# Kernel tuning notes

Hardware: AMD Instinct MI355X
Metric: run time of the kernel (lower is better)

Reference implementation:

```python
import jax, jax.numpy as jnp
import numpy as np

# Enformer/Borzoi-style MHA with relative positional bias
B, T, C = 2, 1536, 1536          # batch, seq bins, input channels
H, K, V = 8, 64, 192             # heads, key_size, value_size
F = 32                           # num_position_features (borzoi, asymmetric: 2 * 16 basis)


def setup_inputs() -> dict:
    key = jax.random.key(0)
    ks = jax.random.split(key, 9)
    he = lambda fan_in: (2.0 / fan_in) ** 0.5  # he_normal scale
    return {
        "x": jax.random.normal(ks[0], (B, T, C), jnp.float32),
        "Wq": jax.random.normal(ks[1], (C, H * K), jnp.float32) * he(C),
        "Wk": jax.random.normal(ks[2], (C, H * K), jnp.float32) * he(C),
        "Wv": jax.random.normal(ks[3], (C, H * V), jnp.float32) * he(C),
        "Wr": jax.random.normal(ks[4], (F, H * K), jnp.float32) * he(F),
        "r_w_bias": jax.random.normal(ks[5], (1, H, 1, K), jnp.float32) * 0.02,
        "r_r_bias": jax.random.normal(ks[6], (1, H, 1, K), jnp.float32) * 0.02,
        "Wo": jax.random.normal(ks[7], (H * V, H * V), jnp.float32) * he(H * V),
        "bo": jnp.zeros((H * V,), jnp.float32),
    }


def positional_features(positions):
    """Borzoi central-mask basis, absolute=True, asymmetric -> [L, F]."""
    nb = F // 2
    pow_rate = np.exp(np.log(T + 1) / nb).astype(np.float32)
    center_widths = pow_rate ** jnp.arange(1, nb + 1, dtype=jnp.float32) - 1.0  # [nb]
    sign = jnp.sign(positions)
    abs_pos = jnp.abs(positions)
    emb = (center_widths[None, :] > abs_pos[:, None]).astype(jnp.float32)  # [L, nb]
    return jnp.concatenate([emb, sign[:, None] * emb], axis=-1)  # [L, 2*nb]


def relative_shift(x):
    """[B,H,T,2T-1] -> [B,H,T,T] relative-shift trick (pad, reshape, slice)."""
    b, h, t, l = x.shape
    x = jnp.pad(x, ((0, 0), (0, 0), (0, 0), (1, 0)))      # [b,h,t,l+1]
    x = x.reshape(b, h, l + 1, t)[:, :, 1:, :]             # [b,h,l,t]
    x = x.reshape(b, h, t, l)
    return x[..., :t]


def reference(x, Wq, Wk, Wv, Wr, r_w_bias, r_r_bias, Wo, bo):
    q = (x @ Wq).reshape(B, T, H, K).transpose(0, 2, 1, 3)   # [B,H,T,K]
    k = (x @ Wk).reshape(B, T, H, K).transpose(0, 2, 1, 3)
    v = (x @ Wv).reshape(B, T, H, V).transpose(0, 2, 1, 3)   # [B,H,T,V]
    q = q * (K ** -0.5)  # scaling=True

    distances = jnp.arange(-T + 1, T, dtype=jnp.float32)     # [2T-1]
    pe = positional_features(distances)                       # [2T-1, F]
    rk = (pe @ Wr).reshape(2 * T - 1, H, K)                   # [2T-1, H, K]

    content_logits = jnp.einsum('bhtk,bhsk->bhts', q + r_w_bias, k)   # [B,H,T,T]
    rel_logits = jnp.einsum('bhtk,rhk->bhtr', q + r_r_bias, rk)       # [B,H,T,2T-1]
    logits = content_logits + relative_shift(rel_logits)

    weights = jax.nn.softmax(logits, axis=-1)
    out = jnp.einsum('bhts,bhsv->bhtv', weights, v)          # [B,H,T,V]
    out = out.transpose(0, 2, 1, 3).reshape(B, T, H * V)     # [B,T,H*V]
    return out @ Wo + bo
```

## Files before the change

### kernel.cpp

```cpp
#include <hip/hip_runtime.h>
#include <hip/hip_bf16.h>

typedef __hip_bfloat16 bf16;
typedef unsigned short ushort;
typedef unsigned int uint;
typedef __attribute__((ext_vector_type(8))) short short8;
typedef __attribute__((ext_vector_type(4))) float f32x4;

#define Bsz 2
#define Tn  1536
#define Cn  1536
#define Hn  8
#define Kn  64
#define Vn  192

__device__ __forceinline__ ushort f2bs(float f) {
  union { bf16 h; ushort u; } cv;
  cv.h = __float2bfloat16(f);
  return cv.u;
}
__device__ __forceinline__ float bs2f(ushort u) {
  union { float f; uint v; } cv; cv.v = ((uint)u) << 16; return cv.f;
}

__device__ __forceinline__ void gld_lds16(const ushort* g, ushort* l) {
  __builtin_amdgcn_global_load_lds(
      (const __attribute__((address_space(1))) uint*)g,
      (__attribute__((address_space(3))) uint*)l, 16, 0, 0);
}

#define DPP_MAXSTEP(x, ctrl)                                                  \
  do {                                                                        \
    union { float f; int i; } a_, b_;                                         \
    a_.f = (x);                                                               \
    b_.i = __builtin_amdgcn_update_dpp(a_.i, a_.i, (ctrl), 0xf, 0xf, true);   \
    (x) = fmaxf((x), b_.f);                                                   \
  } while (0)

__global__ __launch_bounds__(256) void prep(
    const float* __restrict__ x,  const float* __restrict__ Wq,
    const float* __restrict__ Wk, const float* __restrict__ Wv,
    const float* __restrict__ Wo, const float* __restrict__ Wr,
    ushort* __restrict__ xb, ushort* __restrict__ Wt,
    ushort* __restrict__ Wot, ushort* __restrict__ rkdb,
    unsigned char* __restrict__ lutb) {
  const int z = blockIdx.z;
  if (z < 4) {
    if (z < 2 && blockIdx.x >= 16) return;
    const float* in = (z == 0) ? Wq : (z == 1) ? Wk : (z == 2) ? Wv : Wo;
    ushort* out = (z == 0) ? Wt : (z == 1) ? Wt + 512 * 1536
                : (z == 2) ? Wt + 1024 * 1536 : Wot;
    const int Cc = (z < 2) ? 512 : 1536;
    __shared__ float tile[32][33];
    const int bx = blockIdx.x * 32;
    const int by = blockIdx.y * 32;
    const int tx = threadIdx.x & 31, ty = threadIdx.x >> 5;
#pragma unroll
    for (int i = 0; i < 32; i += 8)
      tile[ty + i][tx] = in[(size_t)(by + ty + i) * Cc + bx + tx];
    __syncthreads();
#pragma unroll
    for (int i = 0; i < 32; i += 8)
      out[(size_t)(bx + ty + i) * 1536 + by + tx] = f2bs(tile[tx][ty + i]);
  } else if (z == 4) {
    const int n4 = 3072 * 1536 / 4;
    for (int i = (blockIdx.y * 48 + blockIdx.x) * 256 + threadIdx.x; i < n4;
         i += 2304 * 256) {
      float4 v = ((const float4*)x)[i];
      uint2 o;
      o.x = (uint)f2bs(v.x) | ((uint)f2bs(v.y) << 16);
      o.y = (uint)f2bs(v.z) | ((uint)f2bs(v.w) << 16);
      ((uint2*)xb)[i] = o;
    }
  } else {
    const int base = (blockIdx.y * 48 + blockIdx.x) * 256 + threadIdx.x;
    if (base < 8 * 40 * 64) {
      const int h = base / 2560, rem = base % 2560, u = rem >> 6, k = rem & 63;
      float acc = 0.f;
      if (u < 33) {
        const float sg = (u == 32) ? 0.f : (u < 16 ? 1.f : -1.f);
        const int c = (u == 32) ? 16 : (u < 16 ? u + 1 : u - 15);
#pragma unroll
        for (int i = 0; i < 16; i++)
          if (i >= 16 - c)
            acc += Wr[i * 512 + h * 64 + k] + sg * Wr[(16 + i) * 512 + h * 64 + k];
      }
      rkdb[h * 2560 + u * 64 + k] = f2bs(acc);
    } else if (base < 8 * 40 * 64 + 3072) {
      const int idx = base - 8 * 40 * 64;
      const int d = idx - 1535;
      const float ad = fabsf((float)d);
      int c = 0;
#pragma unroll
      for (int i = 0; i < 16; i++) {
        double cw = exp(log((double)(Tn + 1)) * (double)(i + 1) / 16.0) - 1.0;
        if ((float)cw > ad) c++;
      }
      lutb[idx] = (unsigned char)((d == 0) ? 32 : (d > 0 ? c - 1 : 15 + c));
    }
  }
}

__global__ __launch_bounds__(256) void gemm_qkv(
    const ushort* __restrict__ xb, const ushort* __restrict__ Wt,
    ushort* __restrict__ qb, ushort* __restrict__ kb, ushort* __restrict__ vtb) {
  __shared__ ushort Al[128 * 32];
  __shared__ ushort Bl[128 * 32];
  const int tid = threadIdx.x;
  const int w = tid >> 6, lane = tid & 63, quad = lane >> 4, ln = lane & 15;
  const int bm = blockIdx.y * 128, bn = blockIdx.x * 128;
  const int wm = (w & 1) * 64, wn = (w >> 1) * 64;
  f32x4 acc[4][4];
#pragma unroll
  for (int i = 0; i < 4; i++)
#pragma unroll
    for (int j = 0; j < 4; j++) acc[i][j] = (f32x4){0.f, 0.f, 0.f, 0.f};

  for (int k0 = 0; k0 < 1536; k0 += 32) {
    __syncthreads();
#pragma unroll
    for (int st = 0; st < 2; st++) {
      int idx = tid + st * 256;
      int row = idx >> 2, col = (idx & 3) * 8;
      gld_lds16(xb + (size_t)(bm + row) * 1536 + k0 + col, Al + idx * 8);
      gld_lds16(Wt + (size_t)(bn + row) * 1536 + k0 + col, Bl + idx * 8);
    }
    __syncthreads();
    short8 af[4], bfr[4];
#pragma unroll
    for (int t = 0; t < 4; t++) {
      af[t]  = *(const short8*)(Al + (wm + t * 16 + ln) * 32 + quad * 8);
      bfr[t] = *(const short8*)(Bl + (wn + t * 16 + ln) * 32 + quad * 8);
    }
#pragma unroll
    for (int mt = 0; mt < 4; mt++)
#pragma unroll
      for (int nt = 0; nt < 4; nt++)
        acc[mt][nt] = __builtin_amdgcn_mfma_f32_16x16x32_bf16(
            af[mt], bfr[nt], acc[mt][nt], 0, 0, 0);
  }

  if (bn < 512) {
#pragma unroll
    for (int mt = 0; mt < 4; mt++)
#pragma unroll
      for (int nt = 0; nt < 4; nt++)
#pragma unroll
        for (int r = 0; r < 4; r++) {
          int m = bm + wm + mt * 16 + quad * 4 + r;
          int n = bn + wn + nt * 16 + ln;
          qb[(size_t)m * 512 + n] = f2bs(acc[mt][nt][r] * 0.125f);
        }
  } else if (bn < 1024) {
#pragma unroll
    for (int mt = 0; mt < 4; mt++)
#pragma unroll
      for (int nt = 0; nt < 4; nt++)
#pragma unroll
        for (int r = 0; r < 4; r++) {
          int m = bm + wm + mt * 16 + quad * 4 + r;
          int n = bn - 512 + wn + nt * 16 + ln;
          kb[(size_t)m * 512 + n] = f2bs(acc[mt][nt][r]);
        }
  } else {
#pragma unroll
    for (int mt = 0; mt < 4; mt++)
#pragma unroll
      for (int nt = 0; nt < 4; nt++) {
        int vcol = bn - 1024 + wn + nt * 16 + ln;
        int m0 = bm + wm + mt * 16 + quad * 4;
        uint2 val;
        val.x = (uint)f2bs(acc[mt][nt][0]) | ((uint)f2bs(acc[mt][nt][1]) << 16);
        val.y = (uint)f2bs(acc[mt][nt][2]) | ((uint)f2bs(acc[mt][nt][3]) << 16);
        *(uint2*)(vtb + (size_t)vcol * 3072 + m0) = val;
      }
  }
}

__global__ __launch_bounds__(256) void gemm_out(
    const ushort* __restrict__ att, const ushort* __restrict__ Wot,
    const float* __restrict__ bo, float* __restrict__ out) {
  __shared__ ushort Al[128 * 32];
  __shared__ ushort Bl[128 * 32];
  const int tid = threadIdx.x;
  const int w = tid >> 6, lane = tid & 63, quad = lane >> 4, ln = lane & 15;
  const int bm = blockIdx.y * 128, bn = blockIdx.x * 128;
  const int wm = (w & 1) * 64, wn = (w >> 1) * 64;
  f32x4 acc[4][4];
#pragma unroll
  for (int i = 0; i < 4; i++)
#pragma unroll
    for (int j = 0; j < 4; j++) acc[i][j] = (f32x4){0.f, 0.f, 0.f, 0.f};

  for (int k0 = 0; k0 < 1536; k0 += 32) {
    __syncthreads();
#pragma unroll
    for (int st = 0; st < 2; st++) {
      int idx = tid + st * 256;
      int row = idx >> 2, col = (idx & 3) * 8;
      gld_lds16(att + (size_t)(bm + row) * 1536 + k0 + col, Al + idx * 8);
      gld_lds16(Wot + (size_t)(bn + row) * 1536 + k0 + col, Bl + idx * 8);
    }
    __syncthreads();
    short8 af[4], bfr[4];
#pragma unroll
    for (int t = 0; t < 4; t++) {
      af[t]  = *(const short8*)(Al + (wm + t * 16 + ln) * 32 + quad * 8);
      bfr[t] = *(const short8*)(Bl + (wn + t * 16 + ln) * 32 + quad * 8);
    }
#pragma unroll
    for (int mt = 0; mt < 4; mt++)
#pragma unroll
      for (int nt = 0; nt < 4; nt++)
        acc[mt][nt] = __builtin_amdgcn_mfma_f32_16x16x32_bf16(
            af[mt], bfr[nt], acc[mt][nt], 0, 0, 0);
  }
#pragma unroll
  for (int mt = 0; mt < 4; mt++)
#pragma unroll
    for (int nt = 0; nt < 4; nt++)
#pragma unroll
      for (int r = 0; r < 4; r++) {
        int m = bm + wm + mt * 16 + quad * 4 + r;
        int n = bn + wn + nt * 16 + ln;
        out[(size_t)m * 1536 + n] = acc[mt][nt][r] + bo[n];
      }
}

__global__ __launch_bounds__(256, 3) void attn_mfma(
    const ushort* __restrict__ qb, const ushort* __restrict__ kb,
    const ushort* __restrict__ vtb, const ushort* __restrict__ rkdb,
    const unsigned char* __restrict__ lutb,
    const float* __restrict__ rwb, const float* __restrict__ rrb,
    ushort* __restrict__ op0, ushort* __restrict__ op1,
    float2* __restrict__ mlb) {
  __shared__ __align__(16) char smem[50176];
  ushort* Kl = (ushort*)smem;
  ushort* Vl = (ushort*)(smem + 8192);
  ushort* Dl = (ushort*)(smem + 32768);
  unsigned char* Ll = (unsigned char*)(smem + 37888);

  const int L  = blockIdx.x + 24 * blockIdx.y + 192 * blockIdx.z;
  const int h  = L & 7;
  const int g  = L >> 3;
  const int bsk = g / 24;
  const int b  = bsk >> 1;
  const int sk = bsk & 1;
  const int t0 = (g - bsk * 24) * 64;
  const int bT = b * Tn;
  const int tid = threadIdx.x;
  const int w = tid >> 6, lane = tid & 63, quad = lane >> 4, ln = lane & 15;

  ushort* Pp = (ushort*)(smem + 40960 + w * 2304);

  const int lr  = lane >> 3;
  const int lcx = (lane & 7) ^ lr;

  {
    const int s0 = sk * 768;
#pragma unroll
    for (int i = 0; i < 2; i++) {
      int kc = w * 2 + i, sr = kc * 8 + lr;
      gld_lds16(kb + (size_t)(bT + s0 + sr) * 512 + h * 64 + lcx * 8,
                (ushort*)(smem + kc * 1024) + lane * 8);
    }
#pragma unroll
    for (int i = 0; i < 6; i++) {
      int kc = w * 6 + i, vr = kc * 8 + lr;
      gld_lds16(vtb + (size_t)(h * 192 + vr) * 3072 + bT + s0 + lcx * 8,
                (ushort*)(smem + 8192 + kc * 1024) + lane * 8);
    }
    if (w < 3)
      gld_lds16((const ushort*)(lutb + w * 1024) + lane * 8,
                (ushort*)(smem + 37888 + w * 1024) + lane * 8);
  }

  short8 qw8[2], qr8[2];
  {
    const ushort* qrow = qb + (size_t)(bT + t0 + 16 * w + ln) * 512 + h * 64;
#pragma unroll
    for (int ks = 0; ks < 2; ks++) {
      int k0 = quad * 8 + ks * 32;
#pragma unroll
      for (int e = 0; e < 8; e++) {
        float qv = bs2f(qrow[k0 + e]);
        qw8[ks][e] = (short)f2bs(qv + rwb[h * 64 + k0 + e]);
        qr8[ks][e] = (short)f2bs(qv + rrb[h * 64 + k0 + e]);
      }
    }
  }

  {
    f32x4 Dacc[3];
#pragma unroll
    for (int ut = 0; ut < 3; ut++) {
      Dacc[ut] = (f32x4){0.f, 0.f, 0.f, 0.f};
#pragma unroll
      for (int ks = 0; ks < 2; ks++) {
        int urow = 16 * ut + ln; urow = urow > 39 ? 39 : urow;
        short8 bfr = *(const short8*)(rkdb + h * 2560 + urow * 64 + quad * 8 + ks * 32);
        Dacc[ut] = __builtin_amdgcn_mfma_f32_16x16x32_bf16(qr8[ks], bfr, Dacc[ut], 0, 0, 0);
      }
    }
    const int trow = 16 * w + 4 * quad;
#pragma unroll
    for (int ut = 0; ut < 2; ut++)
#pragma unroll
      for (int r = 0; r < 4; r++)
        Dl[(trow + r) * 40 + 16 * ut + ln] = f2bs(Dacc[ut][r]);
    if (ln == 0) {
#pragma unroll
      for (int r = 0; r < 4; r++)
        Dl[(trow + r) * 40 + 32] = f2bs(Dacc[2][r]);
    }
  }

  f32x4 Oacc[12];
  f32x4 Lacc = (f32x4){0.f, 0.f, 0.f, 0.f};
  float m_i[4];
#pragma unroll
  for (int vt = 0; vt < 12; vt++) Oacc[vt] = (f32x4){0.f, 0.f, 0.f, 0.f};
#pragma unroll
  for (int r = 0; r < 4; r++) m_i[r] = -1e30f;

  short8 ones8;
#pragma unroll
  for (int e = 0; e < 8; e++) ones8[e] = (short)0x3F80;

  __syncthreads();

  const int ibase = sk * 768 - t0 - 16 * w - 4 * quad + ln + 1535;
  const int tl0 = 16 * w + 4 * quad;

  for (int ch = 0; ch < 12; ch++) {
    float dval[4][4];
#pragma unroll
    for (int ct = 0; ct < 4; ct++)
#pragma unroll
      for (int r = 0; r < 4; r++) {
        int idx = ibase + 64 * ch + 16 * ct - r;
        dval[ct][r] = bs2f(Dl[(tl0 + r) * 40 + Ll[idx]]);
      }

    f32x4 Sacc[4];
    __builtin_amdgcn_s_setprio(1);
#pragma unroll
    for (int ct = 0; ct < 4; ct++) {
      Sacc[ct] = (f32x4){0.f, 0.f, 0.f, 0.f};
#pragma unroll
      for (int ks = 0; ks < 2; ks++) {
        short8 bfr = *(const short8*)(
            Kl + (16 * ct + ln) * 64 + ((quad + 4 * ks) ^ (ln & 7)) * 8);
        Sacc[ct] = __builtin_amdgcn_mfma_f32_16x16x32_bf16(qw8[ks], bfr, Sacc[ct], 0, 0, 0);
      }
    }
    __builtin_amdgcn_s_setprio(0);

    float pS[4][4];
#pragma unroll
    for (int ct = 0; ct < 4; ct++)
#pragma unroll
      for (int r = 0; r < 4; r++)
        pS[ct][r] = Sacc[ct][r] + dval[ct][r];

    float alpha[4];
#pragma unroll
    for (int r = 0; r < 4; r++) {
      float mx = fmaxf(fmaxf(pS[0][r], pS[1][r]), fmaxf(pS[2][r], pS[3][r]));
      DPP_MAXSTEP(mx, 0xB1);
      DPP_MAXSTEP(mx, 0x4E);
      DPP_MAXSTEP(mx, 0x124);
      DPP_MAXSTEP(mx, 0x128);
      float mnew = fmaxf(m_i[r], mx);
      alpha[r] = __expf(m_i[r] - mnew);
      m_i[r] = mnew;
#pragma unroll
      for (int ct = 0; ct < 4; ct++)
        pS[ct][r] = __expf(pS[ct][r] - mnew);
    }
#pragma unroll
    for (int vt = 0; vt < 12; vt++)
#pragma unroll
      for (int r = 0; r < 4; r++) Oacc[vt][r] *= alpha[r];
#pragma unroll
    for (int r = 0; r < 4; r++) Lacc[r] *= alpha[r];
#pragma unroll
    for (int ct = 0; ct < 4; ct++)
#pragma unroll
      for (int r = 0; r < 4; r++)
        Pp[(4 * quad + r) * 72 + 16 * ct + ln] = f2bs(pS[ct][r]);
    __asm__ volatile("s_waitcnt lgkmcnt(0)" ::: "memory");
    short8 afr[2];
#pragma unroll
    for (int ks = 0; ks < 2; ks++)
      afr[ks] = *(const short8*)(Pp + ln * 72 + quad * 8 + ks * 32);

    __syncthreads();

    if (ch < 11) {
      const int s0n = sk * 768 + ch * 64 + 64;
#pragma unroll
      for (int i = 0; i < 2; i++) {
        int kc = w * 2 + i, sr = kc * 8 + lr;
        gld_lds16(kb + (size_t)(bT + s0n + sr) * 512 + h * 64 + lcx * 8,
                  (ushort*)(smem + kc * 1024) + lane * 8);
      }
    }

    __builtin_amdgcn_s_setprio(1);
    Lacc = __builtin_amdgcn_mfma_f32_16x16x32_bf16(afr[0], ones8, Lacc, 0, 0, 0);
    Lacc = __builtin_amdgcn_mfma_f32_16x16x32_bf16(afr[1], ones8, Lacc, 0, 0, 0);
#pragma unroll
    for (int vt = 0; vt < 12; vt++) {
#pragma unroll
      for (int ks = 0; ks < 2; ks++) {
        short8 bfr = *(const short8*)(
            Vl + (16 * vt + ln) * 64 + ((quad + 4 * ks) ^ (ln & 7)) * 8);
        Oacc[vt] = __builtin_amdgcn_mfma_f32_16x16x32_bf16(afr[ks], bfr, Oacc[vt], 0, 0, 0);
      }
    }
    __builtin_amdgcn_s_setprio(0);

    __syncthreads();

    if (ch < 11) {
      const int s0n = sk * 768 + ch * 64 + 64;
#pragma unroll
      for (int i = 0; i < 6; i++) {
        int kc = w * 6 + i, vr = kc * 8 + lr;
        gld_lds16(vtb + (size_t)(h * 192 + vr) * 3072 + bT + s0n + lcx * 8,
                  (ushort*)(smem + 8192 + kc * 1024) + lane * 8);
      }
    }
  }

  ushort* op = sk ? op1 : op0;
  float inv[4];
#pragma unroll
  for (int r = 0; r < 4; r++) inv[r] = 1.f / Lacc[r];
#pragma unroll
  for (int vt = 0; vt < 12; vt++)
#pragma unroll
    for (int r = 0; r < 4; r++) {
      int t = t0 + 16 * w + 4 * quad + r;
      op[(size_t)(bT + t) * 1536 + h * 192 + 16 * vt + ln] = f2bs(Oacc[vt][r] * inv[r]);
    }
  if (ln == 0) {
#pragma unroll
    for (int r = 0; r < 4; r++) {
      int t = t0 + 16 * w + 4 * quad + r;
      float2 v; v.x = m_i[r]; v.y = Lacc[r];
      mlb[((sk * 2 + b) * 8 + h) * 1536 + t] = v;
    }
  }
}

__global__ __launch_bounds__(256) void attn_combine(
    const ushort* __restrict__ op0, const ushort* __restrict__ op1,
    const float2* __restrict__ mlb, ushort* __restrict__ att) {
  int g = blockIdx.x * 256 + threadIdx.x;
  int row = g / 384;
  int c4 = (g - row * 384) * 4;
  int b = row >= 1536;
  int t = row - b * 1536;
  int h = c4 / 192;
  float2 ml0 = mlb[((0 + b) * 8 + h) * 1536 + t];
  float2 ml1 = mlb[((2 + b) * 8 + h) * 1536 + t];
  float M = fmaxf(ml0.x, ml1.x);
  float w0 = __expf(ml0.x - M) * ml0.y;
  float w1 = __expf(ml1.x - M) * ml1.y;
  float inv = 1.f / (w0 + w1);
  w0 *= inv; w1 *= inv;
  size_t off = (size_t)row * 1536 + c4;
  uint2 a = *(const uint2*)(op0 + off);
  uint2 c = *(const uint2*)(op1 + off);
  uint2 o;
  float r0 = w0 * bs2f((ushort)(a.x & 0xffff)) + w1 * bs2f((ushort)(c.x & 0xffff));
  float r1 = w0 * bs2f((ushort)(a.x >> 16))    + w1 * bs2f((ushort)(c.x >> 16));
  float r2 = w0 * bs2f((ushort)(a.y & 0xffff)) + w1 * bs2f((ushort)(c.y & 0xffff));
  float r3 = w0 * bs2f((ushort)(a.y >> 16))    + w1 * bs2f((ushort)(c.y >> 16));
  o.x = (uint)f2bs(r0) | ((uint)f2bs(r1) << 16);
  o.y = (uint)f2bs(r2) | ((uint)f2bs(r3) << 16);
  *(uint2*)(att + off) = o;
}

extern "C" void kernel_launch(void* const* d_in, const int* in_sizes, int n_in,
                              void* d_out, int out_size, void* d_ws, size_t ws_size,
                              hipStream_t stream) {
  const float* x   = (const float*)d_in[0];
  const float* Wq  = (const float*)d_in[1];
  const float* Wk  = (const float*)d_in[2];
  const float* Wv  = (const float*)d_in[3];
  const float* Wr  = (const float*)d_in[4];
  const float* rwb = (const float*)d_in[5];
  const float* rrb = (const float*)d_in[6];
  const float* Wo  = (const float*)d_in[7];
  const float* bo  = (const float*)d_in[8];
  float* out = (float*)d_out;

  char* ws = (char*)d_ws;
  ushort* xb  = (ushort*)ws;
  ushort* op1 = (ushort*)ws;
  ushort* att = (ushort*)ws;
  ushort* Wot = (ushort*)(ws + 9437184);
  ushort* Wt  = (ushort*)(ws + 14155776);
  ushort* op0 = (ushort*)(ws + 14155776);
  ushort* qb  = (ushort*)(ws + 23592960);
  ushort* kb  = (ushort*)(ws + 26738688);
  ushort* vtb = (ushort*)(ws + 29884416);
  unsigned char* lutb = (unsigned char*)(ws + 41287680);
  ushort* rkdb = (ushort*)(ws + 41290752);
  float2* mlb = (float2*)(ws + 42467328);

  prep<<<dim3(48, 48, 6), dim3(256), 0, stream>>>(
      x, Wq, Wk, Wv, Wo, Wr, xb, Wt, Wot, rkdb, lutb);
  gemm_qkv<<<dim3(20, 24), dim3(256), 0, stream>>>(xb, Wt, qb, kb, vtb);
  attn_mfma<<<dim3(24, 8, 4), dim3(256), 0, stream>>>(
      qb, kb, vtb, rkdb, lutb, rwb, rrb, op0, op1, mlb);
  attn_combine<<<dim3(4608), dim3(256), 0, stream>>>(op0, op1, mlb, att);
  gemm_out<<<dim3(12, 24), dim3(256), 0, stream>>>(att, Wot, bo, out);
}
```

Before: 224.3 us.

## Fuse split-K combine into output GEMM, remap GEMM blocks, lazy softmax rescale

Removes the separate attn_combine kernel and instead merges the two split-key partial outputs while loading the A tile of the output projection GEMM, saving a launch and a full write/read of the combined attention buffer. Both GEMMs get a remapped block index so that consecutive blocks are spread differently across XCDs/tiles for cache locality. The flash-attention loop skips the running-max rescale of the accumulators unless some row's max grew by more than a threshold of 8, which avoids most rescale multiplies at the risk of larger exponent ranges. The fused GEMM A-load now uses plain register loads and stores to LDS instead of direct global-to-LDS loads.

```diff
diff --git a/kernel.cpp b/kernel.cpp
--- a/kernel.cpp
+++ b/kernel.cpp
@@ -36,6 +36,12 @@
     b_.i = __builtin_amdgcn_update_dpp(a_.i, a_.i, (ctrl), 0xf, 0xf, true);   \
     (x) = fmaxf((x), b_.f);                                                   \
   } while (0)
+
+__device__ __forceinline__ uint cmb2(uint a, uint c, float w0, float w1) {
+  float r0 = w0 * bs2f((ushort)(a & 0xffff)) + w1 * bs2f((ushort)(c & 0xffff));
+  float r1 = w0 * bs2f((ushort)(a >> 16))    + w1 * bs2f((ushort)(c >> 16));
+  return (uint)f2bs(r0) | ((uint)f2bs(r1) << 16);
+}
 
 __global__ __launch_bounds__(256) void prep(
     const float* __restrict__ x,  const float* __restrict__ Wq,
@@ -108,7 +114,9 @@
   __shared__ ushort Bl[128 * 32];
   const int tid = threadIdx.x;
   const int w = tid >> 6, lane = tid & 63, quad = lane >> 4, ln = lane & 15;
-  const int bm = blockIdx.y * 128, bn = blockIdx.x * 128;
+  const int Lb = blockIdx.x + 20 * blockIdx.y;
+  const int wg = (Lb & 7) * 60 + (Lb >> 3);
+  const int bm = (wg % 24) * 128, bn = (wg / 24) * 128;
   const int wm = (w & 1) * 64, wn = (w >> 1) * 64;
   f32x4 acc[4][4];
 #pragma unroll
@@ -178,14 +186,22 @@
 }
 
 __global__ __launch_bounds__(256) void gemm_out(
-    const ushort* __restrict__ att, const ushort* __restrict__ Wot,
+    const ushort* __restrict__ op0, const ushort* __restrict__ op1,
+    const float2* __restrict__ mlb, const ushort* __restrict__ Wot,
     const float* __restrict__ bo, float* __restrict__ out) {
   __shared__ ushort Al[128 * 32];
   __shared__ ushort Bl[128 * 32];
   const int tid = threadIdx.x;
   const int w = tid >> 6, lane = tid & 63, quad = lane >> 4, ln = lane & 15;
-  const int bm = blockIdx.y * 128, bn = blockIdx.x * 128;
+  const int Lb = blockIdx.x + 12 * blockIdx.y;
+  const int wg = (Lb & 7) * 36 + (Lb >> 3);
+  const int bm = (wg % 24) * 128, bn = (wg / 24) * 128;
   const int wm = (w & 1) * 64, wn = (w >> 1) * 64;
+  const int row0 = tid >> 2, col8 = (tid & 3) * 8;
+  const int m0r = bm + row0, m1r = m0r + 64;
+  const int b0 = m0r >= 1536, t0r = m0r - b0 * 1536;
+  const int b1 = m1r >= 1536, t1r = m1r - b1 * 1536;
+  float w00 = 0.f, w01 = 0.f, w10 = 0.f, w11 = 0.f;
   f32x4 acc[4][4];
 #pragma unroll
   for (int i = 0; i < 4; i++)
@@ -193,14 +209,40 @@
     for (int j = 0; j < 4; j++) acc[i][j] = (f32x4){0.f, 0.f, 0.f, 0.f};
 
   for (int k0 = 0; k0 < 1536; k0 += 32) {
-    __syncthreads();
-#pragma unroll
-    for (int st = 0; st < 2; st++) {
-      int idx = tid + st * 256;
-      int row = idx >> 2, col = (idx & 3) * 8;
-      gld_lds16(att + (size_t)(bm + row) * 1536 + k0 + col, Al + idx * 8);
-      gld_lds16(Wot + (size_t)(bn + row) * 1536 + k0 + col, Bl + idx * 8);
-    }
+    if ((k0 % 192) == 0) {
+      const int hh = k0 / 192;
+      float2 ml0 = mlb[((0 + b0) * 8 + hh) * 1536 + t0r];
+      float2 ml1 = mlb[((2 + b0) * 8 + hh) * 1536 + t0r];
+      float M = fmaxf(ml0.x, ml1.x);
+      float a_ = __expf(ml0.x - M) * ml0.y;
+      float c_ = __expf(ml1.x - M) * ml1.y;
+      float inv = 1.f / (a_ + c_);
+      w00 = a_ * inv; w01 = c_ * inv;
+      ml0 = mlb[((0 + b1) * 8 + hh) * 1536 + t1r];
+      ml1 = mlb[((2 + b1) * 8 + hh) * 1536 + t1r];
+      M = fmaxf(ml0.x, ml1.x);
+      a_ = __expf(ml0.x - M) * ml0.y;
+      c_ = __expf(ml1.x - M) * ml1.y;
+      inv = 1.f / (a_ + c_);
+      w10 = a_ * inv; w11 = c_ * inv;
+    }
+    const size_t off0 = (size_t)m0r * 1536 + k0 + col8;
+    const size_t off1 = (size_t)m1r * 1536 + k0 + col8;
+    uint4 a0 = *(const uint4*)(op0 + off0);
+    uint4 c0 = *(const uint4*)(op1 + off0);
+    uint4 a1 = *(const uint4*)(op0 + off1);
+    uint4 c1 = *(const uint4*)(op1 + off1);
+    __syncthreads();
+    uint4 o0, o1;
+    o0.x = cmb2(a0.x, c0.x, w00, w01); o0.y = cmb2(a0.y, c0.y, w00, w01);
+    o0.z = cmb2(a0.z, c0.z, w00, w01); o0.w = cmb2(a0.w, c0.w, w00, w01);
+    *(uint4*)(Al + (size_t)tid * 8) = o0;
+    o1.x = cmb2(a1.x, c1.x, w10, w11); o1.y = cmb2(a1.y, c1.y, w10, w11);
+    o1.z = cmb2(a1.z, c1.z, w10, w11); o1.w = cmb2(a1.w, c1.w, w10, w11);
+    *(uint4*)(Al + (size_t)(tid + 256) * 8) = o1;
+    gld_lds16(Wot + (size_t)(bn + row0) * 1536 + k0 + col8, Bl + tid * 8);
+    gld_lds16(Wot + (size_t)(bn + row0 + 64) * 1536 + k0 + col8,
+              Bl + (tid + 256) * 8);
     __syncthreads();
     short8 af[4], bfr[4];
 #pragma unroll
@@ -363,27 +405,34 @@
       for (int r = 0; r < 4; r++)
         pS[ct][r] = Sacc[ct][r] + dval[ct][r];
 
-    float alpha[4];
+    float mx[4];
 #pragma unroll
     for (int r = 0; r < 4; r++) {
-      float mx = fmaxf(fmaxf(pS[0][r], pS[1][r]), fmaxf(pS[2][r], pS[3][r]));
-      DPP_MAXSTEP(mx, 0xB1);
-      DPP_MAXSTEP(mx, 0x4E);
-      DPP_MAXSTEP(mx, 0x124);
-      DPP_MAXSTEP(mx, 0x128);
-      float mnew = fmaxf(m_i[r], mx);
-      alpha[r] = __expf(m_i[r] - mnew);
-      m_i[r] = mnew;
-#pragma unroll
-      for (int ct = 0; ct < 4; ct++)
-        pS[ct][r] = __expf(pS[ct][r] - mnew);
-    }
-#pragma unroll
-    for (int vt = 0; vt < 12; vt++)
-#pragma unroll
-      for (int r = 0; r < 4; r++) Oacc[vt][r] *= alpha[r];
-#pragma unroll
-    for (int r = 0; r < 4; r++) Lacc[r] *= alpha[r];
+      float m2 = fmaxf(fmaxf(pS[0][r], pS[1][r]), fmaxf(pS[2][r], pS[3][r]));
+      DPP_MAXSTEP(m2, 0xB1);
+      DPP_MAXSTEP(m2, 0x4E);
+      DPP_MAXSTEP(m2, 0x124);
+      DPP_MAXSTEP(m2, 0x128);
+      mx[r] = m2;
+    }
+    int need = (mx[0] > m_i[0] + 8.f) | (mx[1] > m_i[1] + 8.f) |
+               (mx[2] > m_i[2] + 8.f) | (mx[3] > m_i[3] + 8.f);
+    if (__any(need)) {
+#pragma unroll
+      for (int r = 0; r < 4; r++) {
+        float mnew = fmaxf(m_i[r], mx[r]);
+        float alpha = __expf(m_i[r] - mnew);
+        m_i[r] = mnew;
+        Lacc[r] *= alpha;
+#pragma unroll
+        for (int vt = 0; vt < 12; vt++) Oacc[vt][r] *= alpha;
+      }
+    }
+#pragma unroll
+    for (int ct = 0; ct < 4; ct++)
+#pragma unroll
+      for (int r = 0; r < 4; r++)
+        pS[ct][r] = __expf(pS[ct][r] - m_i[r]);
 #pragma unroll
     for (int ct = 0; ct < 4; ct++)
 #pragma unroll
@@ -453,35 +502,6 @@
       mlb[((sk * 2 + b) * 8 + h) * 1536 + t] = v;
     }
   }
-}
-
-__global__ __launch_bounds__(256) void attn_combine(
-    const ushort* __restrict__ op0, const ushort* __restrict__ op1,
-    const float2* __restrict__ mlb, ushort* __restrict__ att) {
-  int g = blockIdx.x * 256 + threadIdx.x;
-  int row = g / 384;
-  int c4 = (g - row * 384) * 4;
-  int b = row >= 1536;
-  int t = row - b * 1536;
-  int h = c4 / 192;
-  float2 ml0 = mlb[((0 + b) * 8 + h) * 1536 + t];
-  float2 ml1 = mlb[((2 + b) * 8 + h) * 1536 + t];
-  float M = fmaxf(ml0.x, ml1.x);
-  float w0 = __expf(ml0.x - M) * ml0.y;
-  float w1 = __expf(ml1.x - M) * ml1.y;
-  float inv = 1.f / (w0 + w1);
-  w0 *= inv; w1 *= inv;
-  size_t off = (size_t)row * 1536 + c4;
-  uint2 a = *(const uint2*)(op0 + off);
-  uint2 c = *(const uint2*)(op1 + off);
-  uint2 o;
-  float r0 = w0 * bs2f((ushort)(a.x & 0xffff)) + w1 * bs2f((ushort)(c.x & 0xffff));
-  float r1 = w0 * bs2f((ushort)(a.x >> 16))    + w1 * bs2f((ushort)(c.x >> 16));
-  float r2 = w0 * bs2f((ushort)(a.y & 0xffff)) + w1 * bs2f((ushort)(c.y & 0xffff));
-  float r3 = w0 * bs2f((ushort)(a.y >> 16))    + w1 * bs2f((ushort)(c.y >> 16));
-  o.x = (uint)f2bs(r0) | ((uint)f2bs(r1) << 16);
-  o.y = (uint)f2bs(r2) | ((uint)f2bs(r3) << 16);
-  *(uint2*)(att + off) = o;
 }
 
 extern "C" void kernel_launch(void* const* d_in, const int* in_sizes, int n_in,
@@ -501,7 +521,6 @@
   char* ws = (char*)d_ws;
   ushort* xb  = (ushort*)ws;
   ushort* op1 = (ushort*)ws;
-  ushort* att = (ushort*)ws;
   ushort* Wot = (ushort*)(ws + 9437184);
   ushort* Wt  = (ushort*)(ws + 14155776);
   ushort* op0 = (ushort*)(ws + 14155776);
@@ -517,6 +536,5 @@
   gemm_qkv<<<dim3(20, 24), dim3(256), 0, stream>>>(xb, Wt, qb, kb, vtb);
   attn_mfma<<<dim3(24, 8, 4), dim3(256), 0, stream>>>(
       qb, kb, vtb, rkdb, lutb, rwb, rrb, op0, op1, mlb);
-  attn_combine<<<dim3(4608), dim3(256), 0, stream>>>(op0, op1, mlb, att);
-  gemm_out<<<dim3(12, 24), dim3(256), 0, stream>>>(att, Wot, bo, out);
-}
+  gemm_out<<<dim3(12, 24), dim3(256), 0, stream>>>(op0, op1, mlb, Wot, bo, out);
+}
```

New measurement: 238.9 us. +6.5%, slower.
